# Performance work log

Measured on AMD Instinct MI355X. Metric: run time of the kernel, lower is better.

Reference implementation:

```python
import jax, jax.numpy as jnp
import numpy as np

N = 50000          # nodes
E = 800000         # random edges (self-loops appended inside reference)
IN = 32            # input feature dim
HID = 128          # hidden dim (heads * per-head channels)
HEADS = 4
CH = HID // HEADS  # 32 per-head channels
OUT = 6
SLOPE = 0.2        # GATv2 leaky_relu negative slope (PyG default)
EPS = 1e-5


def setup_inputs() -> dict:
    key = jax.random.key(0)
    ks = jax.random.split(key, 24)
    def rn(k, shape, scale=0.05):
        return jax.random.normal(k, shape, dtype=jnp.float32) * scale
    return {
        "x": jax.random.normal(ks[0], (N, IN), dtype=jnp.float32),
        "edge_index": jax.random.randint(ks[1], (2, E), 0, N, dtype=jnp.int32),
        # GATv2 layer 1 (separate source/target transforms, share_weights=False)
        "Wl1": rn(ks[2], (IN, HID)), "Wr1": rn(ks[3], (IN, HID)),
        "att1": rn(ks[4], (HEADS, CH)), "bias1": jnp.zeros((HID,), jnp.float32),
        "g1": jnp.ones((HID,), jnp.float32), "b1": jnp.zeros((HID,), jnp.float32),
        # GATv2 layer 2
        "Wl2": rn(ks[5], (HID, HID)), "Wr2": rn(ks[6], (HID, HID)),
        "att2": rn(ks[7], (HEADS, CH)), "bias2": jnp.zeros((HID,), jnp.float32),
        "g2": jnp.ones((HID,), jnp.float32), "b2": jnp.zeros((HID,), jnp.float32),
        # prediction head: Linear(HID, HID//2) -> ReLU -> Linear(HID//2, OUT)
        "Wp1": rn(ks[8], (HID, HID // 2)), "bp1": jnp.zeros((HID // 2,), jnp.float32),
        "Wp2": rn(ks[9], (HID // 2, OUT)), "bp2": jnp.zeros((OUT,), jnp.float32),
        # uncertainty head: Linear(HID, HID//4) -> ReLU -> Linear(HID//4, OUT) -> Softplus
        "Wu1": rn(ks[10], (HID, HID // 4)), "bu1": jnp.zeros((HID // 4,), jnp.float32),
        "Wu2": rn(ks[11], (HID // 4, OUT)), "bu2": jnp.zeros((OUT,), jnp.float32),
    }


def _gatv2(x, src, dst, Wl, Wr, att, bias):
    # GATv2: e_ij = att . leaky_relu(Wl x_j + Wr x_i); softmax over incoming edges of i
    n = x.shape[0]
    xl = (x @ Wl).reshape(n, HEADS, CH)   # source (message) transform
    xr = (x @ Wr).reshape(n, HEADS, CH)   # target transform
    el = xl[src]                           # [E, H, C] gather
    e = jax.nn.leaky_relu(el + xr[dst], SLOPE)
    s = jnp.einsum('ehc,hc->eh', e, att)   # [E, H] attention logits
    m = jax.ops.segment_max(s, dst, num_segments=n)          # stable softmax per dst
    a = jnp.exp(s - m[dst])
    denom = jax.ops.segment_sum(a, dst, num_segments=n)
    alpha = a / denom[dst]                 # [E, H]
    out = jax.ops.segment_sum(el * alpha[:, :, None], dst, num_segments=n)
    return out.reshape(n, HID) + bias


def _ln(h, g, b):
    mu = jnp.mean(h, axis=-1, keepdims=True)
    v = jnp.var(h, axis=-1, keepdims=True)
    return (h - mu) * jax.lax.rsqrt(v + EPS) * g + b


def reference(x, edge_index, Wl1, Wr1, att1, bias1, g1, b1,
              Wl2, Wr2, att2, bias2, g2, b2,
              Wp1, bp1, Wp2, bp2, Wu1, bu1, Wu2, bu2):
    n = x.shape[0]
    loops = jnp.arange(n, dtype=edge_index.dtype)
    ei = jnp.concatenate([edge_index, jnp.stack([loops, loops])], axis=1)
    src, dst = ei[0], ei[1]
    h = _gatv2(x, src, dst, Wl1, Wr1, att1, bias1)
    h = jax.nn.elu(_ln(h, g1, b1))
    h2 = _gatv2(h, src, dst, Wl2, Wr2, att2, bias2)
    h2 = _ln(h2, g2, b2)
    h = jax.nn.elu(h + h2)
    pred = jnp.maximum(h @ Wp1 + bp1, 0.0) @ Wp2 + bp2
    uncertainty = jax.nn.softplus(jnp.maximum(h @ Wu1 + bu1, 0.0) @ Wu2 + bu2)
    return pred, uncertainty
```

## Files before the change

kernel.cpp:

```cpp
#include <hip/hip_runtime.h>
#include <hip/hip_bf16.h>
#include <math.h>

#define HID 128
#define HEADS 4
#define CH 32
#define OUTD 6
#define SLOPE 0.2f
#define LNEPS 1e-5f

static inline int cdiv(int a, int b) { return (a + b - 1) / b; }

__device__ __forceinline__ unsigned short f2bf(float f) {
    unsigned int u = __builtin_bit_cast(unsigned int, f);
    u += 0x7FFFu + ((u >> 16) & 1u);
    return (unsigned short)(u >> 16);
}
__device__ __forceinline__ float bflo(unsigned int u) {
    return __builtin_bit_cast(float, u << 16);
}
__device__ __forceinline__ float bfhi(unsigned int u) {
    return __builtin_bit_cast(float, u & 0xFFFF0000u);
}


__global__ void k_init_deg(int* __restrict__ deg, int n) {
    int i = blockIdx.x * 256 + threadIdx.x;
    if (i < n) deg[i] = 1;
}

__global__ void k_count_rank(const int* __restrict__ ei, int E,
                             int* __restrict__ deg, int* __restrict__ epos) {
    int e = blockIdx.x * 256 + threadIdx.x;
    if (e >= E) return;
    int dst = ei[E + e];
    epos[e] = atomicAdd(&deg[dst], 1);
}

__global__ __launch_bounds__(1024) void k_scan1(const int* __restrict__ deg, int n,
                                                int* __restrict__ ex, int* __restrict__ bsum) {
    __shared__ int sw[16];
    int i = blockIdx.x * 1024 + threadIdx.x;
    int v = (i < n) ? deg[i] : 0;
    int lane = threadIdx.x & 63, w = threadIdx.x >> 6;
    int x = v;
    #pragma unroll
    for (int d = 1; d < 64; d <<= 1) {
        int t = __shfl_up(x, d);
        if (lane >= d) x += t;
    }
    if (lane == 63) sw[w] = x;
    __syncthreads();
    if (w == 0) {
        int t = (lane < 16) ? sw[lane] : 0;
        #pragma unroll
        for (int d = 1; d < 16; d <<= 1) {
            int u = __shfl_up(t, d);
            if (lane >= d) t += u;
        }
        if (lane < 16) sw[lane] = t;
    }
    __syncthreads();
    int woff = (w > 0) ? sw[w - 1] : 0;
    int incl = x + woff;
    if (i < n) ex[i] = incl - v;
    if (threadIdx.x == 1023) bsum[blockIdx.x] = incl;
}

__global__ void k_scan2(int* __restrict__ bsum, int nb) {
    int lane = threadIdx.x;
    int v = (lane < nb) ? bsum[lane] : 0;
    int x = v;
    #pragma unroll
    for (int d = 1; d < 64; d <<= 1) {
        int t = __shfl_up(x, d);
        if (lane >= d) x += t;
    }
    if (lane < nb) bsum[lane] = x - v;
}

__global__ __launch_bounds__(1024) void k_scan3(int* __restrict__ ex, const int* __restrict__ bsum,
                                                int n, int* __restrict__ csr_src) {
    int i = blockIdx.x * 1024 + threadIdx.x;
    if (i < n) {
        int off = ex[i] + bsum[blockIdx.x];
        ex[i] = off;
        csr_src[off] = i;
    }
}

__global__ void k_scatter(const int* __restrict__ ei, const int* __restrict__ epos,
                          const int* __restrict__ offsets, int E,
                          int* __restrict__ csr_src) {
    int e = blockIdx.x * 256 + threadIdx.x;
    if (e >= E) return;
    int src = ei[e], dst = ei[E + e];
    csr_src[offsets[dst] + epos[e]] = src;
}

template <int K>
__global__ __launch_bounds__(128) void dual_linear(const float* __restrict__ X,
                                                   const float* __restrict__ Wl,
                                                   const float* __restrict__ Wr,
                                                   unsigned short* __restrict__ outL,
                                                   unsigned short* __restrict__ outR, int n) {
    __shared__ float sX[32][K + 4];
    int tid = threadIdx.x;
    int tx = tid & 63;
    int ty = tid >> 6;
    int node0 = blockIdx.x * 32;

    constexpr int C4 = K / 4;
    constexpr int NQ = (32 * C4) / 128;
    #pragma unroll
    for (int q = 0; q < NQ; ++q) {
        int g = q * 128 + tid;
        int row = g / C4, c4 = g % C4;
        int gn = node0 + row;
        float4 v = make_float4(0.f, 0.f, 0.f, 0.f);
        if (gn < n) v = *(const float4*)&X[(size_t)gn * K + c4 * 4];
        *(float4*)&sX[row][c4 * 4] = v;
    }
    __syncthreads();

    const float* Wbase = (tx < 32) ? (Wl + tx * 4) : (Wr + (tx - 32) * 4);

    float4 acc[16];
    #pragma unroll
    for (int i = 0; i < 16; ++i) acc[i] = make_float4(0.f, 0.f, 0.f, 0.f);

    #pragma unroll 2
    for (int k4 = 0; k4 < K / 4; ++k4) {
        const float* wp = Wbase + (size_t)k4 * 4 * HID;
        float4 w0 = *(const float4*)(wp);
        float4 w1 = *(const float4*)(wp + HID);
        float4 w2 = *(const float4*)(wp + 2 * HID);
        float4 w3 = *(const float4*)(wp + 3 * HID);
        #pragma unroll
        for (int i = 0; i < 16; ++i) {
            float4 xq = *(const float4*)&sX[ty * 16 + i][k4 * 4];
            acc[i].x = fmaf(xq.x, w0.x, acc[i].x);
            acc[i].y = fmaf(xq.x, w0.y, acc[i].y);
            acc[i].z = fmaf(xq.x, w0.z, acc[i].z);
            acc[i].w = fmaf(xq.x, w0.w, acc[i].w);
            acc[i].x = fmaf(xq.y, w1.x, acc[i].x);
            acc[i].y = fmaf(xq.y, w1.y, acc[i].y);
            acc[i].z = fmaf(xq.y, w1.z, acc[i].z);
            acc[i].w = fmaf(xq.y, w1.w, acc[i].w);
            acc[i].x = fmaf(xq.z, w2.x, acc[i].x);
            acc[i].y = fmaf(xq.z, w2.y, acc[i].y);
            acc[i].z = fmaf(xq.z, w2.z, acc[i].z);
            acc[i].w = fmaf(xq.z, w2.w, acc[i].w);
            acc[i].x = fmaf(xq.w, w3.x, acc[i].x);
            acc[i].y = fmaf(xq.w, w3.y, acc[i].y);
            acc[i].z = fmaf(xq.w, w3.z, acc[i].z);
            acc[i].w = fmaf(xq.w, w3.w, acc[i].w);
        }
    }

    int c = tx * 4;
    unsigned short* basep = (c < HID) ? outL : outR;
    int cc = (c < HID) ? c : c - HID;
    #pragma unroll
    for (int i = 0; i < 16; ++i) {
        int gn = node0 + ty * 16 + i;
        if (gn < n) {
            ushort4 o;
            o.x = f2bf(acc[i].x); o.y = f2bf(acc[i].y);
            o.z = f2bf(acc[i].z); o.w = f2bf(acc[i].w);
            *(ushort4*)&basep[(size_t)gn * HID + cc] = o;
        }
    }
}


struct GatAcc {
    float den;
    float nb[8];
};

template <bool CHECKED>
__device__ __forceinline__ void gat_edge(uint4 r, bool valid,
                                         const float4& xrA, const float4& xrB,
                                         const float4& atA, const float4& atB,
                                         GatAcc& g) {
    float e0 = bflo(r.x), e1 = bfhi(r.x);
    float e2 = bflo(r.y), e3 = bfhi(r.y);
    float e4 = bflo(r.z), e5 = bfhi(r.z);
    float e6 = bflo(r.w), e7 = bfhi(r.w);
    float v0 = e0 + xrA.x; v0 = fmaxf(v0, SLOPE * v0);
    float v1 = e1 + xrA.y; v1 = fmaxf(v1, SLOPE * v1);
    float v2 = e2 + xrA.z; v2 = fmaxf(v2, SLOPE * v2);
    float v3 = e3 + xrA.w; v3 = fmaxf(v3, SLOPE * v3);
    float v4 = e4 + xrB.x; v4 = fmaxf(v4, SLOPE * v4);
    float v5 = e5 + xrB.y; v5 = fmaxf(v5, SLOPE * v5);
    float v6 = e6 + xrB.z; v6 = fmaxf(v6, SLOPE * v6);
    float v7 = e7 + xrB.w; v7 = fmaxf(v7, SLOPE * v7);
    float t = v0 * atA.x;
    t = fmaf(v1, atA.y, t);
    t = fmaf(v2, atA.z, t);
    t = fmaf(v3, atA.w, t);
    t = fmaf(v4, atB.x, t);
    t = fmaf(v5, atB.y, t);
    t = fmaf(v6, atB.z, t);
    t = fmaf(v7, atB.w, t);
    t += __shfl_xor(t, 1);
    t += __shfl_xor(t, 2);
    float a = __expf(t);
    if (CHECKED) a = valid ? a : 0.f;
    g.den += a;
    g.nb[0] = fmaf(a, e0, g.nb[0]);
    g.nb[1] = fmaf(a, e1, g.nb[1]);
    g.nb[2] = fmaf(a, e2, g.nb[2]);
    g.nb[3] = fmaf(a, e3, g.nb[3]);
    g.nb[4] = fmaf(a, e4, g.nb[4]);
    g.nb[5] = fmaf(a, e5, g.nb[5]);
    g.nb[6] = fmaf(a, e6, g.nb[6]);
    g.nb[7] = fmaf(a, e7, g.nb[7]);
}

__global__ __launch_bounds__(256) void gat_aggr(const unsigned short* __restrict__ xl,
                                                const unsigned short* __restrict__ xr,
                                                const int* __restrict__ csr_src,
                                                const int* __restrict__ offsets,
                                                const int* __restrict__ deg,
                                                const float* __restrict__ att,
                                                const float* __restrict__ bias,
                                                const float* __restrict__ gamma,
                                                const float* __restrict__ beta,
                                                const float* __restrict__ hprev,
                                                float* __restrict__ hout,
                                                int n, int layer) {
    int wave = threadIdx.x >> 6;
    int lane = threadIdx.x & 63;
    int dst = blockIdx.x * 4 + wave;
    if (dst >= n) return;

    int lc = lane & 15;
    int eg = lane >> 4;
    int c0 = lc * 8;
    unsigned cb = (unsigned)(lc * 16);

    float4 atA = *(const float4*)&att[c0];
    float4 atB = *(const float4*)&att[c0 + 4];
    const char* xlcb = (const char*)xl + cb;

    uint4 xrr = *(const uint4*)((const char*)xr + (unsigned)dst * 256u + cb);
    float4 xrA = make_float4(bflo(xrr.x), bfhi(xrr.x), bflo(xrr.y), bfhi(xrr.y));
    float4 xrB = make_float4(bflo(xrr.z), bfhi(xrr.z), bflo(xrr.w), bfhi(xrr.w));

    int start = offsets[dst];
    int cnt = deg[dst];
    const int* sp = csr_src + start;

    GatAcc g;
    g.den = 0.f;
    #pragma unroll
    for (int j = 0; j < 8; ++j) g.nb[j] = 0.f;

    for (int base = 0; base < cnt; base += 64) {
        int rem = cnt - base;
        int lim = rem < 64 ? rem : 64;
        int vidx = (lane < lim) ? sp[base + lane] : 0;
        int fq = lim >> 2;
        int q = 0;
        for (; q + 4 <= fq; q += 4) {
            int slot = q * 4 + eg;
            int s0 = __shfl(vidx, slot);
            int s1 = __shfl(vidx, slot + 4);
            int s2 = __shfl(vidx, slot + 8);
            int s3 = __shfl(vidx, slot + 12);
            uint4 r0 = *(const uint4*)(xlcb + ((unsigned)s0 << 8));
            uint4 r1 = *(const uint4*)(xlcb + ((unsigned)s1 << 8));
            uint4 r2 = *(const uint4*)(xlcb + ((unsigned)s2 << 8));
            uint4 r3 = *(const uint4*)(xlcb + ((unsigned)s3 << 8));
            gat_edge<false>(r0, true, xrA, xrB, atA, atB, g);
            gat_edge<false>(r1, true, xrA, xrB, atA, atB, g);
            gat_edge<false>(r2, true, xrA, xrB, atA, atB, g);
            gat_edge<false>(r3, true, xrA, xrB, atA, atB, g);
        }
        for (; q < fq; ++q) {
            int slot = q * 4 + eg;
            int s0 = __shfl(vidx, slot);
            uint4 r0 = *(const uint4*)(xlcb + ((unsigned)s0 << 8));
            gat_edge<false>(r0, true, xrA, xrB, atA, atB, g);
        }
        int tail = lim & 3;
        if (tail) {
            int slot = fq * 4 + eg;
            int s0 = __shfl(vidx, slot);
            uint4 r0 = *(const uint4*)(xlcb + ((unsigned)s0 << 8));
            gat_edge<true>(r0, eg < tail, xrA, xrB, atA, atB, g);
        }
    }

    g.den += __shfl_xor(g.den, 16);
    g.den += __shfl_xor(g.den, 32);
    #pragma unroll
    for (int j = 0; j < 8; ++j) {
        g.nb[j] += __shfl_xor(g.nb[j], 16);
        g.nb[j] += __shfl_xor(g.nb[j], 32);
    }

    float inv = 1.f / g.den;
    float4 bA = *(const float4*)&bias[c0];
    float4 bB = *(const float4*)&bias[c0 + 4];
    float v[8];
    v[0] = fmaf(g.nb[0], inv, bA.x);
    v[1] = fmaf(g.nb[1], inv, bA.y);
    v[2] = fmaf(g.nb[2], inv, bA.z);
    v[3] = fmaf(g.nb[3], inv, bA.w);
    v[4] = fmaf(g.nb[4], inv, bB.x);
    v[5] = fmaf(g.nb[5], inv, bB.y);
    v[6] = fmaf(g.nb[6], inv, bB.z);
    v[7] = fmaf(g.nb[7], inv, bB.w);

    float s1 = 0.f, s2 = 0.f;
    #pragma unroll
    for (int j = 0; j < 8; ++j) {
        s1 += v[j];
        s2 = fmaf(v[j], v[j], s2);
    }
    #pragma unroll
    for (int d = 1; d < 16; d <<= 1) {
        s1 += __shfl_xor(s1, d);
        s2 += __shfl_xor(s2, d);
    }
    float mu = s1 * (1.f / 128.f);
    float var = s2 * (1.f / 128.f) - mu * mu;
    float rs = rsqrtf(var + LNEPS);

    float4 gA = *(const float4*)&gamma[c0];
    float4 gB = *(const float4*)&gamma[c0 + 4];
    float4 beA = *(const float4*)&beta[c0];
    float4 beB = *(const float4*)&beta[c0 + 4];
    float y[8];
    y[0] = (v[0] - mu) * rs * gA.x + beA.x;
    y[1] = (v[1] - mu) * rs * gA.y + beA.y;
    y[2] = (v[2] - mu) * rs * gA.z + beA.z;
    y[3] = (v[3] - mu) * rs * gA.w + beA.w;
    y[4] = (v[4] - mu) * rs * gB.x + beB.x;
    y[5] = (v[5] - mu) * rs * gB.y + beB.y;
    y[6] = (v[6] - mu) * rs * gB.z + beB.z;
    y[7] = (v[7] - mu) * rs * gB.w + beB.w;

    if (layer == 2) {
        const float* hp = &hprev[(size_t)dst * HID + c0];
        float4 hA = *(const float4*)hp;
        float4 hB = *(const float4*)(hp + 4);
        y[0] += hA.x; y[1] += hA.y; y[2] += hA.z; y[3] += hA.w;
        y[4] += hB.x; y[5] += hB.y; y[6] += hB.z; y[7] += hB.w;
    }
    #pragma unroll
    for (int j = 0; j < 8; ++j)
        y[j] = (y[j] > 0.f) ? y[j] : (__expf(y[j]) - 1.f);

    if (eg == 0) {
        float* op = &hout[(size_t)dst * HID + c0];
        *(float4*)op = make_float4(y[0], y[1], y[2], y[3]);
        *(float4*)(op + 4) = make_float4(y[4], y[5], y[6], y[7]);
    }
}

__global__ __launch_bounds__(256) void k_heads(const float* __restrict__ hf,
                                               const float* __restrict__ Wp1, const float* __restrict__ bp1,
                                               const float* __restrict__ Wp2, const float* __restrict__ bp2,
                                               const float* __restrict__ Wu1, const float* __restrict__ bu1,
                                               const float* __restrict__ Wu2, const float* __restrict__ bu2,
                                               float* __restrict__ out, int n) {
    __shared__ float sXH[64 * 132];
    __shared__ float sW[32 * 96];
    __shared__ float sW2[64 * 6 + 32 * 6];
    int tid = threadIdx.x;
    int node0 = blockIdx.x * 64;

    for (int i = tid; i < 576; i += 256) sW2[i] = (i < 384) ? Wp2[i] : Wu2[i - 384];

    {
        int row = tid >> 2, seg = tid & 3;
        int gn = node0 + row;
        const float* src = &hf[(size_t)gn * HID + seg * 32];
        float* dst = &sXH[row * 132 + seg * 32];
        #pragma unroll
        for (int q = 0; q < 8; ++q) {
            float4 v = make_float4(0.f, 0.f, 0.f, 0.f);
            if (gn < n) v = *(const float4*)&src[q * 4];
            *(float4*)&dst[q * 4] = v;
        }
    }

    int cg = tid & 15;
    int ng = tid >> 4;
    int c0 = cg * 6;

    float acc[4][6];
    #pragma unroll
    for (int i = 0; i < 4; ++i)
        #pragma unroll
        for (int j = 0; j < 6; ++j) acc[i][j] = 0.f;

    for (int kc = 0; kc < HID; kc += 32) {
        __syncthreads();
        #pragma unroll
        for (int q = 0; q < 3; ++q) {
            int g = q * 256 + tid;
            int r = g / 24, c4 = g % 24;
            int c = c4 * 4;
            const float* src = (c < 64) ? &Wp1[(size_t)(kc + r) * 64 + c]
                                        : &Wu1[(size_t)(kc + r) * 32 + (c - 64)];
            *(float4*)&sW[r * 96 + c] = *(const float4*)src;
        }
        __syncthreads();
        #pragma unroll
        for (int k = 0; k < 32; ++k) {
            const float* wr = &sW[k * 96 + c0];
            float w0 = wr[0], w1 = wr[1], w2 = wr[2], w3 = wr[3], w4 = wr[4], w5 = wr[5];
            #pragma unroll
            for (int i = 0; i < 4; ++i) {
                float xv = sXH[(ng * 4 + i) * 132 + kc + k];
                acc[i][0] = fmaf(xv, w0, acc[i][0]);
                acc[i][1] = fmaf(xv, w1, acc[i][1]);
                acc[i][2] = fmaf(xv, w2, acc[i][2]);
                acc[i][3] = fmaf(xv, w3, acc[i][3]);
                acc[i][4] = fmaf(xv, w4, acc[i][4]);
                acc[i][5] = fmaf(xv, w5, acc[i][5]);
            }
        }
    }

    __syncthreads();
    float bv[6];
    #pragma unroll
    for (int j = 0; j < 6; ++j) {
        int c = c0 + j;
        bv[j] = (c < 64) ? bp1[c] : bu1[c - 64];
    }
    #pragma unroll
    for (int i = 0; i < 4; ++i) {
        int row = ng * 4 + i;
        #pragma unroll
        for (int j = 0; j < 6; ++j) {
            float v = acc[i][j] + bv[j];
            sXH[row * 97 + c0 + j] = fmaxf(v, 0.f);
        }
    }
    __syncthreads();

    int nl = tid & 63;
    int g = tid >> 6;
    int node = node0 + nl;
    float a0 = 0.f, a1 = 0.f, a2 = 0.f;
    if (g < 2) {
        int j0 = 3 * g;
        const float* hrow = &sXH[nl * 97];
        #pragma unroll 8
        for (int k = 0; k < 64; ++k) {
            float hv = hrow[k];
            a0 = fmaf(hv, sW2[k * 6 + j0], a0);
            a1 = fmaf(hv, sW2[k * 6 + j0 + 1], a1);
            a2 = fmaf(hv, sW2[k * 6 + j0 + 2], a2);
        }
        if (node < n) {
            size_t pb = (size_t)node * 6 + j0;
            out[pb]     = a0 + bp2[j0];
            out[pb + 1] = a1 + bp2[j0 + 1];
            out[pb + 2] = a2 + bp2[j0 + 2];
        }
    } else {
        int j0 = 3 * (g - 2);
        const float* hrow = &sXH[nl * 97 + 64];
        #pragma unroll 8
        for (int k = 0; k < 32; ++k) {
            float hv = hrow[k];
            a0 = fmaf(hv, sW2[384 + k * 6 + j0], a0);
            a1 = fmaf(hv, sW2[384 + k * 6 + j0 + 1], a1);
            a2 = fmaf(hv, sW2[384 + k * 6 + j0 + 2], a2);
        }
        if (node < n) {
            float z0 = a0 + bu2[j0], z1 = a1 + bu2[j0 + 1], z2 = a2 + bu2[j0 + 2];
            size_t ub = (size_t)n * 6 + (size_t)node * 6 + j0;
            out[ub]     = fmaxf(z0, 0.f) + log1pf(__expf(-fabsf(z0)));
            out[ub + 1] = fmaxf(z1, 0.f) + log1pf(__expf(-fabsf(z1)));
            out[ub + 2] = fmaxf(z2, 0.f) + log1pf(__expf(-fabsf(z2)));
        }
    }
}


extern "C" void kernel_launch(void* const* d_in, const int* in_sizes, int n_in,
                              void* d_out, int out_size, void* d_ws, size_t ws_size,
                              hipStream_t stream) {
    const float* x   = (const float*)d_in[0];
    const int*   ei  = (const int*)d_in[1];
    const float* Wl1 = (const float*)d_in[2];
    const float* Wr1 = (const float*)d_in[3];
    const float* att1 = (const float*)d_in[4];
    const float* bias1 = (const float*)d_in[5];
    const float* g1 = (const float*)d_in[6];
    const float* b1 = (const float*)d_in[7];
    const float* Wl2 = (const float*)d_in[8];
    const float* Wr2 = (const float*)d_in[9];
    const float* att2 = (const float*)d_in[10];
    const float* bias2 = (const float*)d_in[11];
    const float* g2 = (const float*)d_in[12];
    const float* b2 = (const float*)d_in[13];
    const float* Wp1 = (const float*)d_in[14];
    const float* bp1 = (const float*)d_in[15];
    const float* Wp2 = (const float*)d_in[16];
    const float* bp2 = (const float*)d_in[17];
    const float* Wu1 = (const float*)d_in[18];
    const float* bu1 = (const float*)d_in[19];
    const float* Wu2 = (const float*)d_in[20];
    const float* bu2 = (const float*)d_in[21];

    int N_ = in_sizes[0] / 32;
    int E_ = in_sizes[1] / 2;
    int EA = E_ + N_;

    char* p = (char*)d_ws;
    size_t fbytes = (size_t)N_ * HID * sizeof(float);
    unsigned short* xl = (unsigned short*)p; p += fbytes / 2;
    unsigned short* xr = (unsigned short*)p; p += fbytes / 2;
    float* h  = (float*)p; p += fbytes;
    float* hf = (float*)p; p += fbytes;
    auto align16 = [](size_t s) { return (s + 15) & ~(size_t)15; };
    int* deg     = (int*)p; p += align16((size_t)N_ * 4);
    int* offsets = (int*)p; p += align16((size_t)N_ * 4);
    int* bsum    = (int*)p; p += 64 * 4;
    int* csr_src = (int*)p; p += align16((size_t)EA * 4);
    int* epos = (int*)hf;

    int nScan = cdiv(N_, 1024);
    k_init_deg<<<cdiv(N_, 256), 256, 0, stream>>>(deg, N_);
    k_count_rank<<<cdiv(E_, 256), 256, 0, stream>>>(ei, E_, deg, epos);
    k_scan1<<<nScan, 1024, 0, stream>>>(deg, N_, offsets, bsum);
    k_scan2<<<1, 64, 0, stream>>>(bsum, nScan);
    k_scan3<<<nScan, 1024, 0, stream>>>(offsets, bsum, N_, csr_src);
    k_scatter<<<cdiv(E_, 256), 256, 0, stream>>>(ei, epos, offsets, E_, csr_src);

    dual_linear<32><<<cdiv(N_, 32), 128, 0, stream>>>(x, Wl1, Wr1, xl, xr, N_);
    gat_aggr<<<cdiv(N_, 4), 256, 0, stream>>>(xl, xr, csr_src, offsets, deg,
                                              att1, bias1, g1, b1, nullptr, h, N_, 1);
    dual_linear<128><<<cdiv(N_, 32), 128, 0, stream>>>(h, Wl2, Wr2, xl, xr, N_);
    gat_aggr<<<cdiv(N_, 4), 256, 0, stream>>>(xl, xr, csr_src, offsets, deg,
                                              att2, bias2, g2, b2, h, hf, N_, 2);
    k_heads<<<cdiv(N_, 64), 256, 0, stream>>>(hf, Wp1, bp1, Wp2, bp2,
                                              Wu1, bu1, Wu2, bu2, (float*)d_out, N_);
}
```

Baseline: 380.6 us.

## Compute dual linear projections with bf16 MFMA and pre-packed weights

Replaces the fp32 FMA dual_linear kernel with an MFMA 16x16x32 bf16 version. Weights are first converted by a small kernel into a packed bf16 layout, inputs are converted to bf16 in shared memory, and results are staged in LDS so they can be written out with coalesced 16-byte stores. The gat_aggr edge loop is also unrolled by 2 instead of 4 to lower register pressure. Rounding inputs to bf16 before the matmul adds a little precision error, and two extra conversion kernels are launched.

```diff
diff --git a/kernel.cpp b/kernel.cpp
--- a/kernel.cpp
+++ b/kernel.cpp
@@ -10,6 +10,9 @@
 #define LNEPS 1e-5f
 
 static inline int cdiv(int a, int b) { return (a + b - 1) / b; }
+
+typedef __bf16 bf16x8 __attribute__((ext_vector_type(8)));
+typedef float f32x4 __attribute__((ext_vector_type(4)));
 
 __device__ __forceinline__ unsigned short f2bf(float f) {
     unsigned int u = __builtin_bit_cast(unsigned int, f);
@@ -98,77 +101,88 @@
     csr_src[offsets[dst] + epos[e]] = src;
 }
 
+__global__ void k_wconv(const float* __restrict__ Wl, const float* __restrict__ Wr,
+                        unsigned short* __restrict__ Wb, int K) {
+    int i = blockIdx.x * 256 + threadIdx.x;
+    if (i >= K * 256) return;
+    int kk = i & 7, c = (i >> 3) & 255, kb = i >> 11;
+    int k = kb * 8 + kk;
+    float v = (c < 128) ? Wl[k * 128 + c] : Wr[k * 128 + (c - 128)];
+    Wb[i] = f2bf(v);
+}
+
 template <int K>
-__global__ __launch_bounds__(128) void dual_linear(const float* __restrict__ X,
-                                                   const float* __restrict__ Wl,
-                                                   const float* __restrict__ Wr,
-                                                   unsigned short* __restrict__ outL,
-                                                   unsigned short* __restrict__ outR, int n) {
-    __shared__ float sX[32][K + 4];
+__global__ __launch_bounds__(256) void dual_linear_mfma(const float* __restrict__ X,
+                                                        const unsigned short* __restrict__ Wb,
+                                                        unsigned short* __restrict__ outL,
+                                                        unsigned short* __restrict__ outR, int n) {
+    constexpr int INS = K + 8;
+    __shared__ unsigned short buf[64 * 264];
     int tid = threadIdx.x;
-    int tx = tid & 63;
-    int ty = tid >> 6;
-    int node0 = blockIdx.x * 32;
-
-    constexpr int C4 = K / 4;
-    constexpr int NQ = (32 * C4) / 128;
-    #pragma unroll
-    for (int q = 0; q < NQ; ++q) {
-        int g = q * 128 + tid;
-        int row = g / C4, c4 = g % C4;
-        int gn = node0 + row;
+    int lane = tid & 63;
+    int w = tid >> 6;
+    int n0 = blockIdx.x * 64;
+
+    constexpr int F4R = K / 4;
+    constexpr int ITS = 64 * F4R / 256;
+    #pragma unroll
+    for (int it = 0; it < ITS; ++it) {
+        int f = it * 256 + tid;
+        int row = f / F4R, c4 = f % F4R;
+        int gn = n0 + row;
         float4 v = make_float4(0.f, 0.f, 0.f, 0.f);
         if (gn < n) v = *(const float4*)&X[(size_t)gn * K + c4 * 4];
-        *(float4*)&sX[row][c4 * 4] = v;
-    }
-    __syncthreads();
-
-    const float* Wbase = (tx < 32) ? (Wl + tx * 4) : (Wr + (tx - 32) * 4);
-
-    float4 acc[16];
-    #pragma unroll
-    for (int i = 0; i < 16; ++i) acc[i] = make_float4(0.f, 0.f, 0.f, 0.f);
-
-    #pragma unroll 2
-    for (int k4 = 0; k4 < K / 4; ++k4) {
-        const float* wp = Wbase + (size_t)k4 * 4 * HID;
-        float4 w0 = *(const float4*)(wp);
-        float4 w1 = *(const float4*)(wp + HID);
-        float4 w2 = *(const float4*)(wp + 2 * HID);
-        float4 w3 = *(const float4*)(wp + 3 * HID);
-        #pragma unroll
-        for (int i = 0; i < 16; ++i) {
-            float4 xq = *(const float4*)&sX[ty * 16 + i][k4 * 4];
-            acc[i].x = fmaf(xq.x, w0.x, acc[i].x);
-            acc[i].y = fmaf(xq.x, w0.y, acc[i].y);
-            acc[i].z = fmaf(xq.x, w0.z, acc[i].z);
-            acc[i].w = fmaf(xq.x, w0.w, acc[i].w);
-            acc[i].x = fmaf(xq.y, w1.x, acc[i].x);
-            acc[i].y = fmaf(xq.y, w1.y, acc[i].y);
-            acc[i].z = fmaf(xq.y, w1.z, acc[i].z);
-            acc[i].w = fmaf(xq.y, w1.w, acc[i].w);
-            acc[i].x = fmaf(xq.z, w2.x, acc[i].x);
-            acc[i].y = fmaf(xq.z, w2.y, acc[i].y);
-            acc[i].z = fmaf(xq.z, w2.z, acc[i].z);
-            acc[i].w = fmaf(xq.z, w2.w, acc[i].w);
-            acc[i].x = fmaf(xq.w, w3.x, acc[i].x);
-            acc[i].y = fmaf(xq.w, w3.y, acc[i].y);
-            acc[i].z = fmaf(xq.w, w3.z, acc[i].z);
-            acc[i].w = fmaf(xq.w, w3.w, acc[i].w);
-        }
-    }
-
-    int c = tx * 4;
-    unsigned short* basep = (c < HID) ? outL : outR;
-    int cc = (c < HID) ? c : c - HID;
-    #pragma unroll
-    for (int i = 0; i < 16; ++i) {
-        int gn = node0 + ty * 16 + i;
+        ushort4 o;
+        o.x = f2bf(v.x); o.y = f2bf(v.y); o.z = f2bf(v.z); o.w = f2bf(v.w);
+        *(ushort4*)&buf[row * INS + c4 * 4] = o;
+    }
+    __syncthreads();
+
+    int l15 = lane & 15, l4 = lane >> 4;
+    int c0 = w * 64;
+
+    f32x4 acc[4][4];
+    #pragma unroll
+    for (int rt = 0; rt < 4; ++rt)
+        #pragma unroll
+        for (int ct = 0; ct < 4; ++ct)
+            acc[rt][ct] = (f32x4)(0.f);
+
+    #pragma unroll
+    for (int ks = 0; ks < K / 32; ++ks) {
+        bf16x8 a[4], b[4];
+        #pragma unroll
+        for (int rt = 0; rt < 4; ++rt)
+            a[rt] = *(const bf16x8*)&buf[(rt * 16 + l15) * INS + ks * 32 + l4 * 8];
+        #pragma unroll
+        for (int ct = 0; ct < 4; ++ct)
+            b[ct] = *(const bf16x8*)&Wb[(((ks * 4 + l4) * 256) + (c0 + ct * 16 + l15)) * 8];
+        #pragma unroll
+        for (int rt = 0; rt < 4; ++rt)
+            #pragma unroll
+            for (int ct = 0; ct < 4; ++ct)
+                acc[rt][ct] = __builtin_amdgcn_mfma_f32_16x16x32_bf16(a[rt], b[ct], acc[rt][ct], 0, 0, 0);
+    }
+    __syncthreads();
+
+    #pragma unroll
+    for (int rt = 0; rt < 4; ++rt)
+        #pragma unroll
+        for (int ct = 0; ct < 4; ++ct)
+            #pragma unroll
+            for (int j = 0; j < 4; ++j)
+                buf[(rt * 16 + l4 * 4 + j) * 264 + c0 + ct * 16 + l15] = f2bf(acc[rt][ct][j]);
+    __syncthreads();
+
+    #pragma unroll
+    for (int it = 0; it < 8; ++it) {
+        int f = it * 256 + tid;
+        int row = f >> 5, cw = f & 31;
+        int gn = n0 + row;
         if (gn < n) {
-            ushort4 o;
-            o.x = f2bf(acc[i].x); o.y = f2bf(acc[i].y);
-            o.z = f2bf(acc[i].z); o.w = f2bf(acc[i].w);
-            *(ushort4*)&basep[(size_t)gn * HID + cc] = o;
+            uint4 v = *(const uint4*)&buf[row * 264 + cw * 8];
+            if (cw < 16) *(uint4*)&outL[(size_t)gn * 128 + cw * 8] = v;
+            else         *(uint4*)&outR[(size_t)gn * 128 + (cw - 16) * 8] = v;
         }
     }
 }
@@ -243,7 +257,7 @@
 
     float4 atA = *(const float4*)&att[c0];
     float4 atB = *(const float4*)&att[c0 + 4];
-    const char* xlcb = (const char*)xl + cb;
+    const char* xlb = (const char*)xl;
 
     uint4 xrr = *(const uint4*)((const char*)xr + (unsigned)dst * 256u + cb);
     float4 xrA = make_float4(bflo(xrr.x), bfhi(xrr.x), bflo(xrr.y), bfhi(xrr.y));
@@ -264,32 +278,26 @@
         int vidx = (lane < lim) ? sp[base + lane] : 0;
         int fq = lim >> 2;
         int q = 0;
-        for (; q + 4 <= fq; q += 4) {
-            int slot = q * 4 + eg;
-            int s0 = __shfl(vidx, slot);
-            int s1 = __shfl(vidx, slot + 4);
-            int s2 = __shfl(vidx, slot + 8);
-            int s3 = __shfl(vidx, slot + 12);
-            uint4 r0 = *(const uint4*)(xlcb + ((unsigned)s0 << 8));
-            uint4 r1 = *(const uint4*)(xlcb + ((unsigned)s1 << 8));
-            uint4 r2 = *(const uint4*)(xlcb + ((unsigned)s2 << 8));
-            uint4 r3 = *(const uint4*)(xlcb + ((unsigned)s3 << 8));
+        for (; q + 2 <= fq; q += 2) {
+            int slot0 = q * 4 + eg;
+            int s0 = __shfl(vidx, slot0);
+            int s1 = __shfl(vidx, slot0 + 4);
+            uint4 r0 = *(const uint4*)(xlb + (((unsigned)s0 << 8) + cb));
+            uint4 r1 = *(const uint4*)(xlb + (((unsigned)s1 << 8) + cb));
             gat_edge<false>(r0, true, xrA, xrB, atA, atB, g);
             gat_edge<false>(r1, true, xrA, xrB, atA, atB, g);
-            gat_edge<false>(r2, true, xrA, xrB, atA, atB, g);
-            gat_edge<false>(r3, true, xrA, xrB, atA, atB, g);
-        }
-        for (; q < fq; ++q) {
-            int slot = q * 4 + eg;
-            int s0 = __shfl(vidx, slot);
-            uint4 r0 = *(const uint4*)(xlcb + ((unsigned)s0 << 8));
+        }
+        if (q < fq) {
+            int slot0 = q * 4 + eg;
+            int s0 = __shfl(vidx, slot0);
+            uint4 r0 = *(const uint4*)(xlb + (((unsigned)s0 << 8) + cb));
             gat_edge<false>(r0, true, xrA, xrB, atA, atB, g);
         }
         int tail = lim & 3;
         if (tail) {
-            int slot = fq * 4 + eg;
-            int s0 = __shfl(vidx, slot);
-            uint4 r0 = *(const uint4*)(xlcb + ((unsigned)s0 << 8));
+            int slot0 = fq * 4 + eg;
+            int s0 = __shfl(vidx, slot0);
+            uint4 r0 = *(const uint4*)(xlb + (((unsigned)s0 << 8) + cb));
             gat_edge<true>(r0, eg < tail, xrA, xrB, atA, atB, g);
         }
     }
@@ -528,6 +536,8 @@
     int* offsets = (int*)p; p += align16((size_t)N_ * 4);
     int* bsum    = (int*)p; p += 64 * 4;
     int* csr_src = (int*)p; p += align16((size_t)EA * 4);
+    unsigned short* Wb1 = (unsigned short*)p; p += 32 * 256 * 2;
+    unsigned short* Wb2 = (unsigned short*)p; p += 128 * 256 * 2;
     int* epos = (int*)hf;
 
     int nScan = cdiv(N_, 1024);
@@ -538,10 +548,13 @@
     k_scan3<<<nScan, 1024, 0, stream>>>(offsets, bsum, N_, csr_src);
     k_scatter<<<cdiv(E_, 256), 256, 0, stream>>>(ei, epos, offsets, E_, csr_src);
 
-    dual_linear<32><<<cdiv(N_, 32), 128, 0, stream>>>(x, Wl1, Wr1, xl, xr, N_);
+    k_wconv<<<cdiv(32 * 256, 256), 256, 0, stream>>>(Wl1, Wr1, Wb1, 32);
+    k_wconv<<<cdiv(128 * 256, 256), 256, 0, stream>>>(Wl2, Wr2, Wb2, 128);
+
+    dual_linear_mfma<32><<<cdiv(N_, 64), 256, 0, stream>>>(x, Wb1, xl, xr, N_);
     gat_aggr<<<cdiv(N_, 4), 256, 0, stream>>>(xl, xr, csr_src, offsets, deg,
                                               att1, bias1, g1, b1, nullptr, h, N_, 1);
-    dual_linear<128><<<cdiv(N_, 32), 128, 0, stream>>>(h, Wl2, Wr2, xl, xr, N_);
+    dual_linear_mfma<128><<<cdiv(N_, 64), 256, 0, stream>>>(h, Wb2, xl, xr, N_);
     gat_aggr<<<cdiv(N_, 4), 256, 0, stream>>>(xl, xr, csr_src, offsets, deg,
                                               att2, bias2, g2, b2, h, hf, N_, 2);
     k_heads<<<cdiv(N_, 64), 256, 0, stream>>>(hf, Wp1, bp1, Wp2, bp2,
```

Measured after the change: 324.3 us. 14.8% less time.
